# Kernel tuning notes

Hardware: AMD Instinct MI355X
Metric: run time of the kernel (lower is better)

The kernel has to match this reference:

```python
import jax, jax.numpy as jnp
import numpy as np

N_NODES = 50000
N_EDGES = 800000
IN_CH, HID_CH, OUT_CH = 128, 128, 64


def setup_inputs() -> dict:
    key = jax.random.key(0)
    k1, k2, k3, k4, k5, k6 = jax.random.split(key, 6)
    x = jax.random.normal(k1, (N_NODES, IN_CH), dtype=jnp.float32)
    edge_index = jax.random.randint(k2, (2, N_EDGES), 0, N_NODES, dtype=jnp.int64)
    # Glorot init like PyG GCNConv; bias zeros-like but random small for test coverage
    s1 = jnp.sqrt(6.0 / (IN_CH + HID_CH)).astype(jnp.float32)
    s2 = jnp.sqrt(6.0 / (HID_CH + OUT_CH)).astype(jnp.float32)
    W1 = jax.random.uniform(k3, (IN_CH, HID_CH), jnp.float32, -s1, s1)
    b1 = jax.random.normal(k4, (HID_CH,), jnp.float32) * 0.01
    W2 = jax.random.uniform(k5, (HID_CH, OUT_CH), jnp.float32, -s2, s2)
    b2 = jax.random.normal(k6, (OUT_CH,), jnp.float32) * 0.01
    return {"x": x, "edge_index": edge_index, "W1": W1, "b1": b1, "W2": W2, "b2": b2}


def gcn_conv(x, edge_index, W, b):
    """PyG GCNConv: add self-loops, symmetric D^-1/2 (A+I) D^-1/2 normalization,
    then aggregate linearly-transformed neighbor features + bias."""
    n = x.shape[0]
    h = x @ W  # [N, F_out]
    src, dst = edge_index[0], edge_index[1]
    # degree counts self-loop (weight 1) plus in-edges at dst
    deg = 1.0 + jax.ops.segment_sum(jnp.ones_like(src, dtype=h.dtype), dst, num_segments=n)
    dinv = jax.lax.rsqrt(deg)  # deg >= 1, no zeros
    norm = dinv[src] * dinv[dst]  # [E]
    agg = jax.ops.segment_sum(h[src] * norm[:, None], dst, num_segments=n)
    # self-loop contribution: norm = dinv[i]*dinv[i] = 1/deg[i]
    return agg + h * (1.0 / deg)[:, None] + b


def reference(x, edge_index, W1, b1, W2, b2):
    # eval-mode forward: dropout is identity
    h = gcn_conv(x, edge_index, W1, b1)
    h = jax.nn.relu(h)
    out = gcn_conv(h, edge_index, W2, b2)
    return out
```

## Files before the change

kernel.cpp:

```cpp
#include <hip/hip_runtime.h>
#include <hip/hip_fp16.h>


typedef _Float16 f16;
typedef __attribute__((ext_vector_type(8))) _Float16 f16x8;
typedef __attribute__((ext_vector_type(4))) float f32x4;

__global__ __launch_bounds__(1024) void scan1_kernel(const int* __restrict__ deg,
                                                     int* __restrict__ rowptr,
                                                     int* __restrict__ bsum,
                                                     float* __restrict__ dinv, int N) {
    __shared__ int wsum[16];
    const int tid = threadIdx.x, lane = tid & 63, wid = tid >> 6;
    const int idx = blockIdx.x * 1024 + tid;
    int v = (idx < N) ? deg[idx] : 0;
    if (idx < N) dinv[idx] = rsqrtf((float)v + 1.0f);
    int incl = v;
#pragma unroll
    for (int off = 1; off < 64; off <<= 1) {
        int t = __shfl_up(incl, off, 64);
        if (lane >= off) incl += t;
    }
    if (lane == 63) wsum[wid] = incl;
    __syncthreads();
    if (wid == 0) {
        int s = (lane < 16) ? wsum[lane] : 0;
#pragma unroll
        for (int off = 1; off < 16; off <<= 1) {
            int t = __shfl_up(s, off, 64);
            if (lane >= off) s += t;
        }
        if (lane < 16) wsum[lane] = s;
    }
    __syncthreads();
    int waveoff = (wid == 0) ? 0 : wsum[wid - 1];
    if (idx < N) rowptr[idx] = waveoff + incl - v;
    if (tid == 1023) bsum[blockIdx.x] = waveoff + incl;
}

__global__ __launch_bounds__(1024) void scan23_kernel(int* __restrict__ rowptr,
                                                      const int* __restrict__ bsum,
                                                      int N, int nb) {
    __shared__ int pfx_s;
    const int tid = threadIdx.x;
    if (tid < 64) {
        int v = (tid < nb && tid < blockIdx.x) ? bsum[tid] : 0;
#pragma unroll
        for (int off = 32; off; off >>= 1) v += __shfl_xor(v, off, 64);
        if (tid == 0) pfx_s = v;
    }
    if (blockIdx.x == 0 && tid >= 64 && tid < 128) {
        int l = tid - 64;
        int v = (l < nb) ? bsum[l] : 0;
#pragma unroll
        for (int off = 32; off; off >>= 1) v += __shfl_xor(v, off, 64);
        if (l == 0) rowptr[N] = v;
    }
    __syncthreads();
    int idx = blockIdx.x * 1024 + tid;
    if (idx < N) rowptr[idx] += pfx_s;
}

__global__ __launch_bounds__(256) void fill_kernel(const int* __restrict__ src,
                                                   const int* __restrict__ dst,
                                                   const int* __restrict__ posw,
                                                   const float* __restrict__ dinv,
                                                   const int* __restrict__ rowptr,
                                                   float2* __restrict__ pairs, int E) {
    int e = blockIdx.x * 256 + threadIdx.x;
    if (e >= E) return;
    int s = src[e], d = dst[e];
    float2 p;
    p.x = __int_as_float(s);
    p.y = dinv[s] * dinv[d];
    pairs[rowptr[d] + posw[e]] = p;
}

template <int KOUT, bool F32IN>
__device__ __forceinline__ void gemm_body(int bid, const void* __restrict__ Xv,
                                          const float* __restrict__ W,
                                          f16* __restrict__ H, int N, f16* Wl) {
    constexpr int CT = KOUT / 16;
    const int tid = threadIdx.x;
    for (int i4 = tid; i4 < 128 * KOUT / 4; i4 += 256) {
        int flat = i4 * 4;
        int k = flat / KOUT, c = flat % KOUT;
        float4 w = *(const float4*)&W[flat];
        Wl[(c + 0) * 136 + k] = (f16)w.x;
        Wl[(c + 1) * 136 + k] = (f16)w.y;
        Wl[(c + 2) * 136 + k] = (f16)w.z;
        Wl[(c + 3) * 136 + k] = (f16)w.w;
    }
    __syncthreads();

    const int lane = tid & 63, wid = tid >> 6;
    const int c = lane & 15, kseg = lane >> 4;
    const int row0 = bid * 64 + wid * 16;
    int arow = row0 + c;
    if (arow >= N) arow = N - 1;

    f32x4 acc[CT];
#pragma unroll
    for (int t = 0; t < CT; ++t) acc[t] = (f32x4){0.f, 0.f, 0.f, 0.f};

#pragma unroll
    for (int kt = 0; kt < 4; ++kt) {
        const int k0 = kt * 32;
        f16x8 a;
        if (F32IN) {
            const float* xp = (const float*)Xv + (long)arow * 128 + k0 + kseg * 8;
            float4 x0 = *(const float4*)xp;
            float4 x1 = *(const float4*)(xp + 4);
            a[0] = (f16)x0.x; a[1] = (f16)x0.y; a[2] = (f16)x0.z; a[3] = (f16)x0.w;
            a[4] = (f16)x1.x; a[5] = (f16)x1.y; a[6] = (f16)x1.z; a[7] = (f16)x1.w;
        } else {
            a = *(const f16x8*)((const f16*)Xv + (long)arow * 128 + k0 + kseg * 8);
        }
#pragma unroll
        for (int ct = 0; ct < CT; ++ct) {
            f16x8 b = *(const f16x8*)&Wl[(ct * 16 + c) * 136 + k0 + kseg * 8];
            acc[ct] = __builtin_amdgcn_mfma_f32_16x16x32_f16(a, b, acc[ct], 0, 0, 0);
        }
    }

    const int rbase = row0 + kseg * 4;
#pragma unroll
    for (int ct = 0; ct < CT; ++ct)
#pragma unroll
        for (int r = 0; r < 4; ++r) {
            int row = rbase + r;
            if (row < N) H[(long)row * KOUT + ct * 16 + c] = (f16)acc[ct][r];
        }
}

template <int KOUT, bool F32IN>
__global__ __launch_bounds__(256) void gemm_kernel(const void* __restrict__ Xv,
                                                   const float* __restrict__ W,
                                                   f16* __restrict__ H, int N) {
    __shared__ f16 Wl[KOUT * 136];
    gemm_body<KOUT, F32IN>(blockIdx.x, Xv, W, H, N, Wl);
}

__global__ __launch_bounds__(256) void deg_gemm_kernel(const int* __restrict__ dst,
                                                       int* __restrict__ deg,
                                                       int* __restrict__ posw, int E,
                                                       const float* __restrict__ x,
                                                       const float* __restrict__ W1,
                                                       f16* __restrict__ h1, int N, int GB) {
    __shared__ f16 Wl[128 * 136];
    if ((int)blockIdx.x < GB) {
        gemm_body<128, true>(blockIdx.x, x, W1, h1, N, Wl);
        return;
    }
    int e = (blockIdx.x - GB) * 256 + threadIdx.x;
    if (e < E) posw[e] = atomicAdd(&deg[dst[e]], 1);
}

template <int STRIDE, int COLOFF, bool RELU, bool OUTF16>
__global__ __launch_bounds__(256) void gather_kernel(const __half* __restrict__ H,
                                                     const int* __restrict__ rowptr,
                                                     const float2* __restrict__ pairs,
                                                     const float* __restrict__ dinv,
                                                     const float* __restrict__ bias,
                                                     void* __restrict__ outv, int N) {
    const int wid = threadIdx.x >> 6;
    const int lane = threadIdx.x & 63;
    const int node = blockIdx.x * 4 + wid;
    if (node >= N) return;
    const int start = rowptr[node], end = rowptr[node + 1];
    const float4* pp4 = (const float4*)pairs;
    const __half* Hh = H + COLOFF + lane;

    float acc = 0.f;
    int e = start;
    if ((e & 1) && e < end) {
        float2 p0 = pairs[e];
        acc += __half2float(Hh[(long)__float_as_int(p0.x) * STRIDE]) * p0.y;
        ++e;
    }
    for (; e + 15 < end; e += 16) {
        float4 q[8];
#pragma unroll
        for (int j = 0; j < 8; ++j) q[j] = pp4[(e >> 1) + j];
        __half uu[16];
#pragma unroll
        for (int j = 0; j < 8; ++j) {
            uu[2 * j]     = Hh[(long)__float_as_int(q[j].x) * STRIDE];
            uu[2 * j + 1] = Hh[(long)__float_as_int(q[j].z) * STRIDE];
        }
#pragma unroll
        for (int j = 0; j < 8; ++j)
            acc += __half2float(uu[2 * j]) * q[j].y + __half2float(uu[2 * j + 1]) * q[j].w;
    }
    for (; e + 3 < end; e += 4) {
        float4 q0 = pp4[e >> 1], q1 = pp4[(e >> 1) + 1];
        float h0 = __half2float(Hh[(long)__float_as_int(q0.x) * STRIDE]);
        float h1 = __half2float(Hh[(long)__float_as_int(q0.z) * STRIDE]);
        float h2 = __half2float(Hh[(long)__float_as_int(q1.x) * STRIDE]);
        float h3 = __half2float(Hh[(long)__float_as_int(q1.z) * STRIDE]);
        acc += h0 * q0.y + h1 * q0.w + h2 * q1.y + h3 * q1.w;
    }
    for (; e < end; ++e) {
        float2 p0 = pairs[e];
        acc += __half2float(Hh[(long)__float_as_int(p0.x) * STRIDE]) * p0.y;
    }
    float di = dinv[node];
    float z = acc + __half2float(Hh[(long)node * STRIDE]) * (di * di) + bias[COLOFF + lane];
    if (RELU) z = fmaxf(z, 0.f);
    if (OUTF16) {
        ((__half*)outv)[(long)node * STRIDE + COLOFF + lane] = __float2half(z);
    } else {
        ((float*)outv)[(long)node * STRIDE + COLOFF + lane] = z;
    }
}

extern "C" void kernel_launch(void* const* d_in, const int* in_sizes, int n_in,
                              void* d_out, int out_size, void* d_ws, size_t ws_size,
                              hipStream_t stream) {
    const float* x  = (const float*)d_in[0];
    const int*   ei = (const int*)d_in[1];
    const float* W1 = (const float*)d_in[2];
    const float* b1 = (const float*)d_in[3];
    const float* W2 = (const float*)d_in[4];
    const float* b2 = (const float*)d_in[5];
    float* out = (float*)d_out;

    const int N = in_sizes[0] / 128;
    const int E = in_sizes[1] / 2;
    const int* src = ei;
    const int* dst = ei + E;
    const int NB = (N + 1023) / 1024;

    float* ws = (float*)d_ws;
    float2* pairs = (float2*)ws;
    long off = 2L * E;
    int* posw   = (int*)(ws + off); off += E;
    int* deg    = (int*)(ws + off); off += N;
    int* rowptr = (int*)(ws + off); off += N + 1;
    int* bsum   = (int*)(ws + off); off += 64;
    float* dinv = ws + off;        off += N;
    off = (off + 3) & ~3L;
    f16* h1 = (f16*)(ws + off); off += (long)N * 64;
    f16* z1 = (f16*)(ws + off); off += (long)N * 64;
    f16* h2 = (f16*)(ws + off); off += (long)N * 32;

    const int GB = (N + 63) / 64;
    const int DB = (E + 255) / 256;

    hipMemsetAsync(deg, 0, (size_t)N * sizeof(int), stream);
    deg_gemm_kernel<<<GB + DB, 256, 0, stream>>>(dst, deg, posw, E, x, W1, h1, N, GB);
    scan1_kernel<<<NB, 1024, 0, stream>>>(deg, rowptr, bsum, dinv, N);
    scan23_kernel<<<NB, 1024, 0, stream>>>(rowptr, bsum, N, NB);
    fill_kernel<<<(E + 255) / 256, 256, 0, stream>>>(src, dst, posw, dinv, rowptr, pairs, E);

    gather_kernel<128, 0, true, true><<<(N + 3) / 4, 256, 0, stream>>>(
        (const __half*)h1, rowptr, pairs, dinv, b1, z1, N);
    gather_kernel<128, 64, true, true><<<(N + 3) / 4, 256, 0, stream>>>(
        (const __half*)h1, rowptr, pairs, dinv, b1, z1, N);

    gemm_kernel<64, false><<<(N + 63) / 64, 256, 0, stream>>>(z1, W2, h2, N);
    gather_kernel<64, 0, false, false><<<(N + 3) / 4, 256, 0, stream>>>(
        (const __half*)h2, rowptr, pairs, dinv, b2, out, N);
}
```

Before: 253.1 us.

## Replace scan with atomic rowptr allocation, fuse fill with GEMM, half2 gather

Replaces the two-kernel prefix scan with a single kernel that hands out row offsets through an atomicAdd on a global counter, and uses deg instead of rowptr[n+1] for segment ends. The CSR fill is moved into the layer-1 GEMM launch so the two overlap. The first-layer gather now processes all 128 columns in one pass with half2 loads instead of two 64-column passes. This removes launches and redundant pair reads, but the row order becomes nondeterministic and locality of the pairs array may suffer.

```diff
diff --git a/kernel.cpp b/kernel.cpp
--- a/kernel.cpp
+++ b/kernel.cpp
@@ -6,74 +6,23 @@
 typedef __attribute__((ext_vector_type(8))) _Float16 f16x8;
 typedef __attribute__((ext_vector_type(4))) float f32x4;
 
-__global__ __launch_bounds__(1024) void scan1_kernel(const int* __restrict__ deg,
+__global__ __launch_bounds__(256) void deg_pos_kernel(const int* __restrict__ dst,
+                                                      int* __restrict__ deg,
+                                                      int* __restrict__ posw, int E) {
+    int e = blockIdx.x * 256 + threadIdx.x;
+    if (e < E) posw[e] = atomicAdd(&deg[dst[e]], 1);
+}
+
+__global__ __launch_bounds__(256) void rowptr_kernel(const int* __restrict__ deg,
                                                      int* __restrict__ rowptr,
-                                                     int* __restrict__ bsum,
+                                                     int* __restrict__ counter,
                                                      float* __restrict__ dinv, int N) {
-    __shared__ int wsum[16];
-    const int tid = threadIdx.x, lane = tid & 63, wid = tid >> 6;
-    const int idx = blockIdx.x * 1024 + tid;
-    int v = (idx < N) ? deg[idx] : 0;
-    if (idx < N) dinv[idx] = rsqrtf((float)v + 1.0f);
-    int incl = v;
-#pragma unroll
-    for (int off = 1; off < 64; off <<= 1) {
-        int t = __shfl_up(incl, off, 64);
-        if (lane >= off) incl += t;
-    }
-    if (lane == 63) wsum[wid] = incl;
-    __syncthreads();
-    if (wid == 0) {
-        int s = (lane < 16) ? wsum[lane] : 0;
-#pragma unroll
-        for (int off = 1; off < 16; off <<= 1) {
-            int t = __shfl_up(s, off, 64);
-            if (lane >= off) s += t;
-        }
-        if (lane < 16) wsum[lane] = s;
-    }
-    __syncthreads();
-    int waveoff = (wid == 0) ? 0 : wsum[wid - 1];
-    if (idx < N) rowptr[idx] = waveoff + incl - v;
-    if (tid == 1023) bsum[blockIdx.x] = waveoff + incl;
-}
-
-__global__ __launch_bounds__(1024) void scan23_kernel(int* __restrict__ rowptr,
-                                                      const int* __restrict__ bsum,
-                                                      int N, int nb) {
-    __shared__ int pfx_s;
-    const int tid = threadIdx.x;
-    if (tid < 64) {
-        int v = (tid < nb && tid < blockIdx.x) ? bsum[tid] : 0;
-#pragma unroll
-        for (int off = 32; off; off >>= 1) v += __shfl_xor(v, off, 64);
-        if (tid == 0) pfx_s = v;
-    }
-    if (blockIdx.x == 0 && tid >= 64 && tid < 128) {
-        int l = tid - 64;
-        int v = (l < nb) ? bsum[l] : 0;
-#pragma unroll
-        for (int off = 32; off; off >>= 1) v += __shfl_xor(v, off, 64);
-        if (l == 0) rowptr[N] = v;
-    }
-    __syncthreads();
-    int idx = blockIdx.x * 1024 + tid;
-    if (idx < N) rowptr[idx] += pfx_s;
-}
-
-__global__ __launch_bounds__(256) void fill_kernel(const int* __restrict__ src,
-                                                   const int* __restrict__ dst,
-                                                   const int* __restrict__ posw,
-                                                   const float* __restrict__ dinv,
-                                                   const int* __restrict__ rowptr,
-                                                   float2* __restrict__ pairs, int E) {
-    int e = blockIdx.x * 256 + threadIdx.x;
-    if (e >= E) return;
-    int s = src[e], d = dst[e];
-    float2 p;
-    p.x = __int_as_float(s);
-    p.y = dinv[s] * dinv[d];
-    pairs[rowptr[d] + posw[e]] = p;
+    int i = blockIdx.x * 256 + threadIdx.x;
+    if (i < N) {
+        int d = deg[i];
+        dinv[i] = rsqrtf((float)d + 1.0f);
+        rowptr[i] = atomicAdd(counter, d);
+    }
 }
 
 template <int KOUT, bool F32IN>
@@ -141,24 +90,33 @@
     gemm_body<KOUT, F32IN>(blockIdx.x, Xv, W, H, N, Wl);
 }
 
-__global__ __launch_bounds__(256) void deg_gemm_kernel(const int* __restrict__ dst,
-                                                       int* __restrict__ deg,
-                                                       int* __restrict__ posw, int E,
-                                                       const float* __restrict__ x,
-                                                       const float* __restrict__ W1,
-                                                       f16* __restrict__ h1, int N, int GB) {
+__global__ __launch_bounds__(256) void fill_gemm_kernel(const int* __restrict__ src,
+                                                        const int* __restrict__ dst,
+                                                        const int* __restrict__ posw,
+                                                        const float* __restrict__ dinv,
+                                                        const int* __restrict__ rowptr,
+                                                        float2* __restrict__ pairs, int E,
+                                                        const float* __restrict__ x,
+                                                        const float* __restrict__ W1,
+                                                        f16* __restrict__ h1, int N, int GB) {
     __shared__ f16 Wl[128 * 136];
     if ((int)blockIdx.x < GB) {
         gemm_body<128, true>(blockIdx.x, x, W1, h1, N, Wl);
         return;
     }
     int e = (blockIdx.x - GB) * 256 + threadIdx.x;
-    if (e < E) posw[e] = atomicAdd(&deg[dst[e]], 1);
-}
-
-template <int STRIDE, int COLOFF, bool RELU, bool OUTF16>
-__global__ __launch_bounds__(256) void gather_kernel(const __half* __restrict__ H,
+    if (e >= E) return;
+    int s = src[e], d = dst[e];
+    float2 p;
+    p.x = __int_as_float(s);
+    p.y = dinv[s] * dinv[d];
+    pairs[rowptr[d] + posw[e]] = p;
+}
+
+template <int F, bool RELU, bool OUTF16>
+__global__ __launch_bounds__(256) void gather_kernel(const void* __restrict__ Hv,
                                                      const int* __restrict__ rowptr,
+                                                     const int* __restrict__ deg,
                                                      const float2* __restrict__ pairs,
                                                      const float* __restrict__ dinv,
                                                      const float* __restrict__ bias,
@@ -167,50 +125,108 @@
     const int lane = threadIdx.x & 63;
     const int node = blockIdx.x * 4 + wid;
     if (node >= N) return;
-    const int start = rowptr[node], end = rowptr[node + 1];
+    const int start = rowptr[node];
+    const int end = start + deg[node];
     const float4* pp4 = (const float4*)pairs;
-    const __half* Hh = H + COLOFF + lane;
-
-    float acc = 0.f;
+    constexpr int SHIFT = (F == 128) ? 8 : 7;
+    const char* Hb = (const char*)Hv + lane * (F == 128 ? 4 : 2);
+
+    float ax = 0.f, ay = 0.f;
     int e = start;
     if ((e & 1) && e < end) {
         float2 p0 = pairs[e];
-        acc += __half2float(Hh[(long)__float_as_int(p0.x) * STRIDE]) * p0.y;
+        uint o = (uint)__float_as_int(p0.x) << SHIFT;
+        if (F == 128) {
+            float2 f0 = __half22float2(*(const __half2*)(Hb + o));
+            ax += f0.x * p0.y; ay += f0.y * p0.y;
+        } else {
+            ax += __half2float(*(const __half*)(Hb + o)) * p0.y;
+        }
         ++e;
     }
     for (; e + 15 < end; e += 16) {
         float4 q[8];
 #pragma unroll
         for (int j = 0; j < 8; ++j) q[j] = pp4[(e >> 1) + j];
-        __half uu[16];
+        uint off[16];
 #pragma unroll
         for (int j = 0; j < 8; ++j) {
-            uu[2 * j]     = Hh[(long)__float_as_int(q[j].x) * STRIDE];
-            uu[2 * j + 1] = Hh[(long)__float_as_int(q[j].z) * STRIDE];
-        }
-#pragma unroll
-        for (int j = 0; j < 8; ++j)
-            acc += __half2float(uu[2 * j]) * q[j].y + __half2float(uu[2 * j + 1]) * q[j].w;
+            off[2 * j]     = (uint)__float_as_int(q[j].x) << SHIFT;
+            off[2 * j + 1] = (uint)__float_as_int(q[j].z) << SHIFT;
+        }
+        if (F == 128) {
+            __half2 uu[16];
+#pragma unroll
+            for (int j = 0; j < 16; ++j) uu[j] = *(const __half2*)(Hb + off[j]);
+#pragma unroll
+            for (int j = 0; j < 8; ++j) {
+                float2 f0 = __half22float2(uu[2 * j]);
+                float2 f1 = __half22float2(uu[2 * j + 1]);
+                ax += f0.x * q[j].y + f1.x * q[j].w;
+                ay += f0.y * q[j].y + f1.y * q[j].w;
+            }
+        } else {
+            __half uu[16];
+#pragma unroll
+            for (int j = 0; j < 16; ++j) uu[j] = *(const __half*)(Hb + off[j]);
+#pragma unroll
+            for (int j = 0; j < 8; ++j)
+                ax += __half2float(uu[2 * j]) * q[j].y + __half2float(uu[2 * j + 1]) * q[j].w;
+        }
     }
     for (; e + 3 < end; e += 4) {
         float4 q0 = pp4[e >> 1], q1 = pp4[(e >> 1) + 1];
-        float h0 = __half2float(Hh[(long)__float_as_int(q0.x) * STRIDE]);
-        float h1 = __half2float(Hh[(long)__float_as_int(q0.z) * STRIDE]);
-        float h2 = __half2float(Hh[(long)__float_as_int(q1.x) * STRIDE]);
-        float h3 = __half2float(Hh[(long)__float_as_int(q1.z) * STRIDE]);
-        acc += h0 * q0.y + h1 * q0.w + h2 * q1.y + h3 * q1.w;
+        uint o0 = (uint)__float_as_int(q0.x) << SHIFT;
+        uint o1 = (uint)__float_as_int(q0.z) << SHIFT;
+        uint o2 = (uint)__float_as_int(q1.x) << SHIFT;
+        uint o3 = (uint)__float_as_int(q1.z) << SHIFT;
+        if (F == 128) {
+            __half2 u0 = *(const __half2*)(Hb + o0);
+            __half2 u1 = *(const __half2*)(Hb + o1);
+            __half2 u2 = *(const __half2*)(Hb + o2);
+            __half2 u3 = *(const __half2*)(Hb + o3);
+            float2 f0 = __half22float2(u0), f1 = __half22float2(u1);
+            float2 f2 = __half22float2(u2), f3 = __half22float2(u3);
+            ax += f0.x * q0.y + f1.x * q0.w + f2.x * q1.y + f3.x * q1.w;
+            ay += f0.y * q0.y + f1.y * q0.w + f2.y * q1.y + f3.y * q1.w;
+        } else {
+            float h0 = __half2float(*(const __half*)(Hb + o0));
+            float h1 = __half2float(*(const __half*)(Hb + o1));
+            float h2 = __half2float(*(const __half*)(Hb + o2));
+            float h3 = __half2float(*(const __half*)(Hb + o3));
+            ax += h0 * q0.y + h1 * q0.w + h2 * q1.y + h3 * q1.w;
+        }
     }
     for (; e < end; ++e) {
         float2 p0 = pairs[e];
-        acc += __half2float(Hh[(long)__float_as_int(p0.x) * STRIDE]) * p0.y;
-    }
+        uint o = (uint)__float_as_int(p0.x) << SHIFT;
+        if (F == 128) {
+            float2 f0 = __half22float2(*(const __half2*)(Hb + o));
+            ax += f0.x * p0.y; ay += f0.y * p0.y;
+        } else {
+            ax += __half2float(*(const __half*)(Hb + o)) * p0.y;
+        }
+    }
+
     float di = dinv[node];
-    float z = acc + __half2float(Hh[(long)node * STRIDE]) * (di * di) + bias[COLOFF + lane];
-    if (RELU) z = fmaxf(z, 0.f);
-    if (OUTF16) {
-        ((__half*)outv)[(long)node * STRIDE + COLOFF + lane] = __float2half(z);
+    float d2 = di * di;
+    if (F == 128) {
+        float2 fs = __half22float2(*(const __half2*)(Hb + ((uint)node << SHIFT)));
+        float2 bz = ((const float2*)bias)[lane];
+        float zx = ax + fs.x * d2 + bz.x;
+        float zy = ay + fs.y * d2 + bz.y;
+        if (RELU) { zx = fmaxf(zx, 0.f); zy = fmaxf(zy, 0.f); }
+        if (OUTF16) {
+            ((__half2*)outv)[(long)node * 64 + lane] = __float22half2_rn(make_float2(zx, zy));
+        } else {
+            float2 o = {zx, zy};
+            ((float2*)outv)[(long)node * 64 + lane] = o;
+        }
     } else {
-        ((float*)outv)[(long)node * STRIDE + COLOFF + lane] = z;
+        float z = ax + __half2float(*(const __half*)(Hb + ((uint)node << SHIFT))) * d2 + bias[lane];
+        if (RELU) z = fmaxf(z, 0.f);
+        if (OUTF16) ((__half*)outv)[(long)node * 64 + lane] = __float2half(z);
+        else        ((float*)outv)[(long)node * 64 + lane] = z;
     }
 }
 
@@ -229,36 +245,33 @@
     const int E = in_sizes[1] / 2;
     const int* src = ei;
     const int* dst = ei + E;
-    const int NB = (N + 1023) / 1024;
 
     float* ws = (float*)d_ws;
     float2* pairs = (float2*)ws;
     long off = 2L * E;
-    int* posw   = (int*)(ws + off); off += E;
-    int* deg    = (int*)(ws + off); off += N;
-    int* rowptr = (int*)(ws + off); off += N + 1;
-    int* bsum   = (int*)(ws + off); off += 64;
-    float* dinv = ws + off;        off += N;
+    int* posw    = (int*)(ws + off); off += E;
+    int* deg     = (int*)(ws + off); off += N;
+    int* counter = (int*)(ws + off); off += 1;
+    int* rowptr  = (int*)(ws + off); off += N;
+    float* dinv  = ws + off;        off += N;
     off = (off + 3) & ~3L;
     f16* h1 = (f16*)(ws + off); off += (long)N * 64;
     f16* z1 = (f16*)(ws + off); off += (long)N * 64;
     f16* h2 = (f16*)(ws + off); off += (long)N * 32;
 
     const int GB = (N + 63) / 64;
-    const int DB = (E + 255) / 256;
-
-    hipMemsetAsync(deg, 0, (size_t)N * sizeof(int), stream);
-    deg_gemm_kernel<<<GB + DB, 256, 0, stream>>>(dst, deg, posw, E, x, W1, h1, N, GB);
-    scan1_kernel<<<NB, 1024, 0, stream>>>(deg, rowptr, bsum, dinv, N);
-    scan23_kernel<<<NB, 1024, 0, stream>>>(rowptr, bsum, N, NB);
-    fill_kernel<<<(E + 255) / 256, 256, 0, stream>>>(src, dst, posw, dinv, rowptr, pairs, E);
-
-    gather_kernel<128, 0, true, true><<<(N + 3) / 4, 256, 0, stream>>>(
-        (const __half*)h1, rowptr, pairs, dinv, b1, z1, N);
-    gather_kernel<128, 64, true, true><<<(N + 3) / 4, 256, 0, stream>>>(
-        (const __half*)h1, rowptr, pairs, dinv, b1, z1, N);
+    const int FB = (E + 255) / 256;
+
+    hipMemsetAsync(deg, 0, (size_t)(N + 1) * sizeof(int), stream);
+    deg_pos_kernel<<<FB, 256, 0, stream>>>(dst, deg, posw, E);
+    rowptr_kernel<<<(N + 255) / 256, 256, 0, stream>>>(deg, rowptr, counter, dinv, N);
+    fill_gemm_kernel<<<GB + FB, 256, 0, stream>>>(src, dst, posw, dinv, rowptr, pairs, E,
+                                                  x, W1, h1, N, GB);
+
+    gather_kernel<128, true, true><<<(N + 3) / 4, 256, 0, stream>>>(
+        h1, rowptr, deg, pairs, dinv, b1, z1, N);
 
     gemm_kernel<64, false><<<(N + 63) / 64, 256, 0, stream>>>(z1, W2, h2, N);
-    gather_kernel<64, 0, false, false><<<(N + 3) / 4, 256, 0, stream>>>(
-        (const __half*)h2, rowptr, pairs, dinv, b2, out, N);
-}
+    gather_kernel<64, false, false><<<(N + 3) / 4, 256, 0, stream>>>(
+        h2, rowptr, deg, pairs, dinv, b2, out, N);
+}
```

Measured after the change: 240.4 us. -5.0%, faster.

## Shard layer-1 gather by column groups and fuse fill with first GEMM

Applied to the files above, without the earlier changes.

The layer-1 aggregation now runs as one kernel instead of two column-half passes. Blocks are sharded into 8 column groups of 16 halves each, with lanes split across 8 edges and 8 half2 columns, and partial sums are reduced by shuffles. The idea is that each shard's slice of h1 stays cache-resident while the shard is processed. The degree-count atomics move to their own kernel, and the CSR fill is fused with the first GEMM so they overlap. The trade-off is narrower 4-byte gathers and more shuffle reductions per node, and the edge list is re-read 8 times.

```diff
diff --git a/kernel.cpp b/kernel.cpp
--- a/kernel.cpp
+++ b/kernel.cpp
@@ -5,6 +5,13 @@
 typedef _Float16 f16;
 typedef __attribute__((ext_vector_type(8))) _Float16 f16x8;
 typedef __attribute__((ext_vector_type(4))) float f32x4;
+
+__global__ __launch_bounds__(256) void deg_pos_kernel(const int* __restrict__ dst,
+                                                      int* __restrict__ deg,
+                                                      int* __restrict__ posw, int E) {
+    int e = blockIdx.x * 256 + threadIdx.x;
+    if (e < E) posw[e] = atomicAdd(&deg[dst[e]], 1);
+}
 
 __global__ __launch_bounds__(1024) void scan1_kernel(const int* __restrict__ deg,
                                                      int* __restrict__ rowptr,
@@ -59,21 +66,6 @@
     __syncthreads();
     int idx = blockIdx.x * 1024 + tid;
     if (idx < N) rowptr[idx] += pfx_s;
-}
-
-__global__ __launch_bounds__(256) void fill_kernel(const int* __restrict__ src,
-                                                   const int* __restrict__ dst,
-                                                   const int* __restrict__ posw,
-                                                   const float* __restrict__ dinv,
-                                                   const int* __restrict__ rowptr,
-                                                   float2* __restrict__ pairs, int E) {
-    int e = blockIdx.x * 256 + threadIdx.x;
-    if (e >= E) return;
-    int s = src[e], d = dst[e];
-    float2 p;
-    p.x = __int_as_float(s);
-    p.y = dinv[s] * dinv[d];
-    pairs[rowptr[d] + posw[e]] = p;
 }
 
 template <int KOUT, bool F32IN>
@@ -141,41 +133,98 @@
     gemm_body<KOUT, F32IN>(blockIdx.x, Xv, W, H, N, Wl);
 }
 
-__global__ __launch_bounds__(256) void deg_gemm_kernel(const int* __restrict__ dst,
-                                                       int* __restrict__ deg,
-                                                       int* __restrict__ posw, int E,
-                                                       const float* __restrict__ x,
-                                                       const float* __restrict__ W1,
-                                                       f16* __restrict__ h1, int N, int GB) {
+__global__ __launch_bounds__(256) void fill_gemm_kernel(const int* __restrict__ src,
+                                                        const int* __restrict__ dst,
+                                                        const int* __restrict__ posw,
+                                                        const float* __restrict__ dinv,
+                                                        const int* __restrict__ rowptr,
+                                                        float2* __restrict__ pairs, int E,
+                                                        const float* __restrict__ x,
+                                                        const float* __restrict__ W1,
+                                                        f16* __restrict__ h1, int N, int GB) {
     __shared__ f16 Wl[128 * 136];
     if ((int)blockIdx.x < GB) {
         gemm_body<128, true>(blockIdx.x, x, W1, h1, N, Wl);
         return;
     }
     int e = (blockIdx.x - GB) * 256 + threadIdx.x;
-    if (e < E) posw[e] = atomicAdd(&deg[dst[e]], 1);
-}
-
-template <int STRIDE, int COLOFF, bool RELU, bool OUTF16>
-__global__ __launch_bounds__(256) void gather_kernel(const __half* __restrict__ H,
-                                                     const int* __restrict__ rowptr,
-                                                     const float2* __restrict__ pairs,
-                                                     const float* __restrict__ dinv,
-                                                     const float* __restrict__ bias,
-                                                     void* __restrict__ outv, int N) {
+    if (e >= E) return;
+    int s = src[e], d = dst[e];
+    float2 p;
+    p.x = __int_as_float(s);
+    p.y = dinv[s] * dinv[d];
+    pairs[rowptr[d] + posw[e]] = p;
+}
+
+__global__ __launch_bounds__(256) void gather128_shard_kernel(const __half2* __restrict__ Hu,
+                                                              const int* __restrict__ rowptr,
+                                                              const float2* __restrict__ pairs,
+                                                              const float* __restrict__ dinv,
+                                                              const float* __restrict__ b1,
+                                                              __half2* __restrict__ z1, int N) {
+    const int g = blockIdx.x & 7;
+    const int tile = blockIdx.x >> 3;
+    const int tid = threadIdx.x;
+    const int wid = tid >> 6, lane = tid & 63;
+    const int es = lane >> 3;
+    const int c = lane & 7;
+    const int col = g * 8 + c;
+    const float2 bz = ((const float2*)b1)[col];
+
+    const int node0 = tile * 32 + wid * 8;
+#pragma unroll 1
+    for (int nn = 0; nn < 8; ++nn) {
+        const int node = node0 + nn;
+        if (node >= N) return;
+        const int start = rowptr[node], end = rowptr[node + 1];
+
+        float ax = 0.f, ay = 0.f;
+        int e = start;
+        for (; e + 7 < end; e += 8) {
+            float2 p = pairs[e + es];
+            float2 f = __half22float2(Hu[(long)__float_as_int(p.x) * 64 + col]);
+            ax += f.x * p.y;
+            ay += f.y * p.y;
+        }
+        if (e + es < end) {
+            float2 p = pairs[e + es];
+            float2 f = __half22float2(Hu[(long)__float_as_int(p.x) * 64 + col]);
+            ax += f.x * p.y;
+            ay += f.y * p.y;
+        }
+        ax += __shfl_xor(ax, 8);  ay += __shfl_xor(ay, 8);
+        ax += __shfl_xor(ax, 16); ay += __shfl_xor(ay, 16);
+        ax += __shfl_xor(ax, 32); ay += __shfl_xor(ay, 32);
+
+        if (es == 0) {
+            float di = dinv[node];
+            float d2 = di * di;
+            float2 fs = __half22float2(Hu[(long)node * 64 + col]);
+            float zx = fmaxf(ax + fs.x * d2 + bz.x, 0.f);
+            float zy = fmaxf(ay + fs.y * d2 + bz.y, 0.f);
+            z1[(long)node * 64 + col] = __float22half2_rn(make_float2(zx, zy));
+        }
+    }
+}
+
+__global__ __launch_bounds__(256) void gather64_kernel(const __half* __restrict__ H,
+                                                       const int* __restrict__ rowptr,
+                                                       const float2* __restrict__ pairs,
+                                                       const float* __restrict__ dinv,
+                                                       const float* __restrict__ bias,
+                                                       float* __restrict__ out, int N) {
     const int wid = threadIdx.x >> 6;
     const int lane = threadIdx.x & 63;
     const int node = blockIdx.x * 4 + wid;
     if (node >= N) return;
     const int start = rowptr[node], end = rowptr[node + 1];
     const float4* pp4 = (const float4*)pairs;
-    const __half* Hh = H + COLOFF + lane;
 
     float acc = 0.f;
     int e = start;
     if ((e & 1) && e < end) {
         float2 p0 = pairs[e];
-        acc += __half2float(Hh[(long)__float_as_int(p0.x) * STRIDE]) * p0.y;
+        acc += __half2float(H[(long)__float_as_int(p0.x) * 64 + lane]) * p0.y;
         ++e;
     }
     for (; e + 15 < end; e += 16) {
@@ -185,8 +234,8 @@
         __half uu[16];
 #pragma unroll
         for (int j = 0; j < 8; ++j) {
-            uu[2 * j]     = Hh[(long)__float_as_int(q[j].x) * STRIDE];
-            uu[2 * j + 1] = Hh[(long)__float_as_int(q[j].z) * STRIDE];
+            uu[2 * j]     = H[(long)__float_as_int(q[j].x) * 64 + lane];
+            uu[2 * j + 1] = H[(long)__float_as_int(q[j].z) * 64 + lane];
         }
 #pragma unroll
         for (int j = 0; j < 8; ++j)
@@ -194,24 +243,19 @@
     }
     for (; e + 3 < end; e += 4) {
         float4 q0 = pp4[e >> 1], q1 = pp4[(e >> 1) + 1];
-        float h0 = __half2float(Hh[(long)__float_as_int(q0.x) * STRIDE]);
-        float h1 = __half2float(Hh[(long)__float_as_int(q0.z) * STRIDE]);
-        float h2 = __half2float(Hh[(long)__float_as_int(q1.x) * STRIDE]);
-        float h3 = __half2float(Hh[(long)__float_as_int(q1.z) * STRIDE]);
+        float h0 = __half2float(H[(long)__float_as_int(q0.x) * 64 + lane]);
+        float h1 = __half2float(H[(long)__float_as_int(q0.z) * 64 + lane]);
+        float h2 = __half2float(H[(long)__float_as_int(q1.x) * 64 + lane]);
+        float h3 = __half2float(H[(long)__float_as_int(q1.z) * 64 + lane]);
         acc += h0 * q0.y + h1 * q0.w + h2 * q1.y + h3 * q1.w;
     }
     for (; e < end; ++e) {
         float2 p0 = pairs[e];
-        acc += __half2float(Hh[(long)__float_as_int(p0.x) * STRIDE]) * p0.y;
+        acc += __half2float(H[(long)__float_as_int(p0.x) * 64 + lane]) * p0.y;
     }
     float di = dinv[node];
-    float z = acc + __half2float(Hh[(long)node * STRIDE]) * (di * di) + bias[COLOFF + lane];
-    if (RELU) z = fmaxf(z, 0.f);
-    if (OUTF16) {
-        ((__half*)outv)[(long)node * STRIDE + COLOFF + lane] = __float2half(z);
-    } else {
-        ((float*)outv)[(long)node * STRIDE + COLOFF + lane] = z;
-    }
+    float z = acc + __half2float(H[(long)node * 64 + lane]) * (di * di) + bias[lane];
+    out[(long)node * 64 + lane] = z;
 }
 
 extern "C" void kernel_launch(void* const* d_in, const int* in_sizes, int n_in,
@@ -245,20 +289,23 @@
     f16* h2 = (f16*)(ws + off); off += (long)N * 32;
 
     const int GB = (N + 63) / 64;
-    const int DB = (E + 255) / 256;
+    const int FB = (E + 255) / 256;
 
     hipMemsetAsync(deg, 0, (size_t)N * sizeof(int), stream);
-    deg_gemm_kernel<<<GB + DB, 256, 0, stream>>>(dst, deg, posw, E, x, W1, h1, N, GB);
+    deg_pos_kernel<<<FB, 256, 0, stream>>>(dst, deg, posw, E);
     scan1_kernel<<<NB, 1024, 0, stream>>>(deg, rowptr, bsum, dinv, N);
     scan23_kernel<<<NB, 1024, 0, stream>>>(rowptr, bsum, N, NB);
-    fill_kernel<<<(E + 255) / 256, 256, 0, stream>>>(src, dst, posw, dinv, rowptr, pairs, E);
-
-    gather_kernel<128, 0, true, true><<<(N + 3) / 4, 256, 0, stream>>>(
-        (const __half*)h1, rowptr, pairs, dinv, b1, z1, N);
-    gather_kernel<128, 64, true, true><<<(N + 3) / 4, 256, 0, stream>>>(
-        (const __half*)h1, rowptr, pairs, dinv, b1, z1, N);
+
+    fill_gemm_kernel<<<GB + FB, 256, 0, stream>>>(src, dst, posw, dinv, rowptr, pairs, E,
+                                                  x, W1, h1, N, GB);
+
+    {
+        const int tiles = (N + 31) / 32;
+        gather128_shard_kernel<<<tiles * 8, 256, 0, stream>>>(
+            (const __half2*)h1, rowptr, pairs, dinv, b1, (__half2*)z1, N);
+    }
 
     gemm_kernel<64, false><<<(N + 63) / 64, 256, 0, stream>>>(z1, W2, h2, N);
-    gather_kernel<64, 0, false, false><<<(N + 3) / 4, 256, 0, stream>>>(
+    gather64_kernel<<<(N + 3) / 4, 256, 0, stream>>>(
         (const __half*)h2, rowptr, pairs, dinv, b2, out, N);
 }
```

Measured after the change: 345.4 us. 1.36x slower.
